# Kernel tuning notes

Hardware: AMD Instinct MI355X
Metric: run time of the kernel (lower is better)

Reference implementation:

```python
import jax, jax.numpy as jnp
import numpy as np

NUM_HEADS = 8
LN_EPS = 1e-5


def setup_inputs() -> dict:
    key = jax.random.key(0)
    ks = jax.random.split(key, 12)
    N, H, G = 100000, 512, 256
    s = 1.0 / np.sqrt(H)
    return {
        "x": jax.random.normal(ks[0], (N, H), dtype=jnp.float32),
        "batch": jnp.sort(jax.random.randint(ks[1], (N,), 0, G)),
        "query": jax.random.normal(ks[2], (H,), dtype=jnp.float32),
        "k_w": jax.random.uniform(ks[3], (H, H), minval=-s, maxval=s, dtype=jnp.float32),
        "k_b": jax.random.uniform(ks[4], (H,), minval=-s, maxval=s, dtype=jnp.float32),
        "v_w": jax.random.uniform(ks[5], (H, H), minval=-s, maxval=s, dtype=jnp.float32),
        "v_b": jax.random.uniform(ks[6], (H,), minval=-s, maxval=s, dtype=jnp.float32),
        "o_w": jax.random.uniform(ks[7], (H, H), minval=-s, maxval=s, dtype=jnp.float32),
        "o_b": jax.random.uniform(ks[8], (H,), minval=-s, maxval=s, dtype=jnp.float32),
        "ln_g": jnp.ones((H,), dtype=jnp.float32),
        "ln_b": jnp.zeros((H,), dtype=jnp.float32),
        "num_graphs": 256,
    }


def reference(x, batch, query, k_w, k_b, v_w, v_b, o_w, o_b, ln_g, ln_b, num_graphs):
    N, H = x.shape
    nh = NUM_HEADS
    hd = H // nh
    # projections (torch Linear: x @ W.T + b)
    k = (x @ k_w.T + k_b).reshape(N, nh, hd)
    v = (x @ v_w.T + v_b).reshape(N, nh, hd)
    q = query.reshape(nh, hd)
    # per-node, per-head attention logits against the shared graph query
    s = jnp.einsum("nhd,hd->nh", k, q) / np.float32(np.sqrt(hd))  # [N, nh]
    # segment softmax over nodes of each graph (stable via segment max)
    s_max = jax.ops.segment_max(s, batch, num_segments=num_graphs)  # [G, nh]
    w = jnp.exp(s - s_max[batch])  # [N, nh]
    denom = jax.ops.segment_sum(w, batch, num_segments=num_graphs)  # [G, nh]
    numer = jax.ops.segment_sum(w[:, :, None] * v, batch, num_segments=num_graphs)  # [G, nh, hd]
    attended = numer / jnp.where(denom > 0, denom, 1.0)[:, :, None]  # zeros for empty graphs
    out = attended.reshape(num_graphs, H)
    out = out @ o_w.T + o_b
    # layer norm over last dim
    mu = out.mean(-1, keepdims=True)
    var = out.var(-1, keepdims=True)
    out = (out - mu) / jnp.sqrt(var + LN_EPS) * ln_g + ln_b
    return out
```

## Files before the change

kernel.cpp:

```cpp
#include <hip/hip_runtime.h>
#include <math.h>

#define H 512
#define NH 8
#define NG 256
#define SPLIT 4

#define WS_QK   0
#define WS_SB   4096
#define WS_SEG  4352
#define WS_VWT  8192
#define WS_OWT  270336
#define WS_TP   532480
#define WS_DP   4726784


__global__ __launch_bounds__(256) void k_setup(
    const int* __restrict__ batch, int N, int* __restrict__ seg,
    const float* __restrict__ k_w, const float* __restrict__ k_b,
    const float* __restrict__ query, float* __restrict__ qk, float* __restrict__ sb,
    const float* __restrict__ vw, const float* __restrict__ ow,
    float* __restrict__ vwt, float* __restrict__ owt) {
  __shared__ float tile[32][33];
  const int b = blockIdx.x;
  if (b < 2) {
    int g = b * 256 + threadIdx.x;
    if (g > NG) return;
    int lo = 0, hi = N;
    while (lo < hi) { int mid = (lo + hi) >> 1; if (batch[mid] < g) lo = mid + 1; else hi = mid; }
    seg[g] = lo;
  } else if (b < 18) {
    int gt = (b - 2) * 256 + threadIdx.x;
    int h = gt >> 9, j = gt & 511;
    float a = 0.f;
#pragma unroll 8
    for (int d = 0; d < 64; ++d)
      a = fmaf(k_w[(size_t)(h * 64 + d) * H + j], query[h * 64 + d], a);
    qk[j * 8 + h] = a * 0.125f;
    if (gt < 8) {
      float s = 0.f;
      for (int d = 0; d < 64; ++d) s = fmaf(k_b[gt * 64 + d], query[gt * 64 + d], s);
      sb[gt] = s * 0.125f;
    }
  } else {
    int bb = b - 18;
    const float* in  = (bb < 256) ? vw  : ow;
    float*       out = (bb < 256) ? vwt : owt;
    int tidx = bb & 255;
    int bx = tidx & 15, by = tidx >> 4;
    int tx = threadIdx.x & 31, ty = threadIdx.x >> 5;
#pragma unroll
    for (int k = 0; k < 4; ++k)
      tile[ty + 8 * k][tx] = in[(size_t)(by * 32 + ty + 8 * k) * H + bx * 32 + tx];
    __syncthreads();
#pragma unroll
    for (int k = 0; k < 4; ++k)
      out[(size_t)(bx * 32 + ty + 8 * k) * H + by * 32 + tx] = tile[tx][ty + 8 * k];
  }
}


#define DPP_ADD(v, ctrl, rmask)                                                   \
  v += __int_as_float(__builtin_amdgcn_update_dpp(0, __float_as_int(v), ctrl,     \
                                                  rmask, 0xf, true))

__global__ __launch_bounds__(256, 2) void k_main(
    const float* __restrict__ x, const float* __restrict__ qk, const float* __restrict__ sb,
    const int* __restrict__ seg, float* __restrict__ T_part, float* __restrict__ den_part) {
  const int g = blockIdx.x >> 2, p = blockIdx.x & (SPLIT - 1);
  const int s0 = seg[g], e0 = seg[g + 1], len = e0 - s0;
  const int na = s0 + (len * p) / SPLIT;
  const int nb = s0 + (len * (p + 1)) / SPLIT;
  const int lane = threadIdx.x & 63, wid = threadIdx.x >> 6;

  float qk_r[8][8];
#pragma unroll
  for (int ci = 0; ci < 8; ++ci) {
    int j = (ci < 4) ? (4 * lane + ci) : (256 + 4 * lane + ci - 4);
    const float4* row = (const float4*)(qk + j * 8);
    float4 q0 = row[0], q1 = row[1];
    qk_r[ci][0] = q0.x; qk_r[ci][1] = q0.y; qk_r[ci][2] = q0.z; qk_r[ci][3] = q0.w;
    qk_r[ci][4] = q1.x; qk_r[ci][5] = q1.y; qk_r[ci][6] = q1.z; qk_r[ci][7] = q1.w;
  }
  float sbr[8];
#pragma unroll
  for (int h = 0; h < 8; ++h) sbr[h] = sb[h];

  float T_r[8][8];
  float den[8];
#pragma unroll
  for (int h = 0; h < 8; ++h) {
    den[h] = 0.f;
#pragma unroll
    for (int ci = 0; ci < 8; ++ci) T_r[h][ci] = 0.f;
  }

  const float4* x4 = (const float4*)x;
  int n = na + wid;
  float4 b0a, b0b, b1a, b1b;
  if (n < nb)     { size_t a = (size_t)n * 128 + lane;       b0a = x4[a]; b0b = x4[a + 64]; }
  if (n + 4 < nb) { size_t a = (size_t)(n + 4) * 128 + lane; b1a = x4[a]; b1b = x4[a + 64]; }

  for (; n < nb; n += 4) {
    float4 b2a, b2b;
    if (n + 8 < nb) { size_t a = (size_t)(n + 8) * 128 + lane; b2a = x4[a]; b2b = x4[a + 64]; }

    float xv[8] = {b0a.x, b0a.y, b0a.z, b0a.w, b0b.x, b0b.y, b0b.z, b0b.w};
    float pp[8] = {0.f, 0.f, 0.f, 0.f, 0.f, 0.f, 0.f, 0.f};
#pragma unroll
    for (int ci = 0; ci < 8; ++ci)
#pragma unroll
      for (int h = 0; h < 8; ++h) pp[h] = fmaf(xv[ci], qk_r[ci][h], pp[h]);

#pragma unroll
    for (int h = 0; h < 8; ++h) DPP_ADD(pp[h], 0x111, 0xf);
#pragma unroll
    for (int h = 0; h < 8; ++h) DPP_ADD(pp[h], 0x112, 0xf);
#pragma unroll
    for (int h = 0; h < 8; ++h) DPP_ADD(pp[h], 0x114, 0xf);
#pragma unroll
    for (int h = 0; h < 8; ++h) DPP_ADD(pp[h], 0x118, 0xf);
#pragma unroll
    for (int h = 0; h < 8; ++h) DPP_ADD(pp[h], 0x142, 0xa);
#pragma unroll
    for (int h = 0; h < 8; ++h) DPP_ADD(pp[h], 0x143, 0xc);

    float w[8];
#pragma unroll
    for (int h = 0; h < 8; ++h) {
      float s = __int_as_float(__builtin_amdgcn_readlane(__float_as_int(pp[h]), 63));
      w[h] = __expf(s + sbr[h]);
      den[h] += w[h];
    }
#pragma unroll
    for (int h = 0; h < 8; ++h)
#pragma unroll
      for (int ci = 0; ci < 8; ++ci) T_r[h][ci] = fmaf(w[h], xv[ci], T_r[h][ci]);

    b0a = b1a; b0b = b1b; b1a = b2a; b1b = b2b;
  }

  __shared__ float T_lds[8][512];
  __shared__ float den_lds[4][8];
  for (int wv = 0; wv < 4; ++wv) {
    if (wid == wv) {
#pragma unroll
      for (int h = 0; h < 8; ++h) {
        float4 v0 = make_float4(T_r[h][0], T_r[h][1], T_r[h][2], T_r[h][3]);
        float4 v1 = make_float4(T_r[h][4], T_r[h][5], T_r[h][6], T_r[h][7]);
        float4* d0 = (float4*)&T_lds[h][4 * lane];
        float4* d1 = (float4*)&T_lds[h][256 + 4 * lane];
        if (wv == 0) { *d0 = v0; *d1 = v1; }
        else {
          float4 o0 = *d0, o1 = *d1;
          o0.x += v0.x; o0.y += v0.y; o0.z += v0.z; o0.w += v0.w;
          o1.x += v1.x; o1.y += v1.y; o1.z += v1.z; o1.w += v1.w;
          *d0 = o0; *d1 = o1;
        }
      }
      if (lane == 0) {
#pragma unroll
        for (int h = 0; h < 8; ++h) den_lds[wv][h] = den[h];
      }
    }
    __syncthreads();
  }
  const int gp = blockIdx.x;
  float4* Tp4 = (float4*)(T_part + (size_t)gp * (NH * H));
  const float4* Tl4 = (const float4*)T_lds;
  for (int k = threadIdx.x; k < NH * H / 4; k += 256) Tp4[k] = Tl4[k];
  if (threadIdx.x < 8) {
    float d = den_lds[0][threadIdx.x] + den_lds[1][threadIdx.x] +
              den_lds[2][threadIdx.x] + den_lds[3][threadIdx.x];
    den_part[gp * 8 + threadIdx.x] = d;
  }
}


__global__ __launch_bounds__(512) void k_epi(
    const float* __restrict__ T_part, const float* __restrict__ den_part,
    const float* __restrict__ vwt, const float* __restrict__ vb,
    const float* __restrict__ owt, const float* __restrict__ ob,
    const float* __restrict__ lng, const float* __restrict__ lnb,
    float* __restrict__ out) {
  const int g0 = blockIdx.x * 2;
  const int t = threadIdx.x;
  __shared__ float Tl[2][NH * H];
  __shared__ float att[2][H];
  __shared__ float den_s[2][8], dinv_s[2][8];
  __shared__ float red[2][2][8];

#pragma unroll
  for (int gi = 0; gi < 2; ++gi) {
    const float4* tp = (const float4*)(T_part + (size_t)(g0 + gi) * SPLIT * (NH * H));
    float4* tl4 = (float4*)Tl[gi];
    for (int k = t; k < NH * H / 4; k += 512) {
      float4 acc = tp[k];
#pragma unroll
      for (int p = 1; p < SPLIT; ++p) {
        float4 v = tp[p * (NH * H / 4) + k];
        acc.x += v.x; acc.y += v.y; acc.z += v.z; acc.w += v.w;
      }
      tl4[k] = acc;
    }
  }
  if (t < 16) {
    int gi = t >> 3, h = t & 7;
    float d = 0.f;
#pragma unroll
    for (int p = 0; p < SPLIT; ++p) d += den_part[((g0 + gi) * SPLIT + p) * 8 + h];
    den_s[gi][h] = d;
    dinv_s[gi][h] = (d > 0.f) ? 1.f / d : 1.f;
  }
  __syncthreads();

  {
    const int h = t >> 6;
    const float* T0 = &Tl[0][h * H];
    const float* T1 = &Tl[1][h * H];
    float a0 = 0.f, a1 = 0.f;
#pragma unroll 8
    for (int j = 0; j < H; ++j) {
      float wv_ = vwt[(size_t)j * H + t];
      a0 = fmaf(T0[j], wv_, a0);
      a1 = fmaf(T1[j], wv_, a1);
    }
    att[0][t] = (a0 + den_s[0][h] * vb[t]) * dinv_s[0][h];
    att[1][t] = (a1 + den_s[1][h] * vb[t]) * dinv_s[1][h];
  }
  __syncthreads();

  float o0 = ob[t], o1 = o0;
#pragma unroll 8
  for (int k = 0; k < H; ++k) {
    float w_ = owt[(size_t)k * H + t];
    o0 = fmaf(att[0][k], w_, o0);
    o1 = fmaf(att[1][k], w_, o1);
  }

  float r10 = o0, r20 = o0 * o0, r11 = o1, r21 = o1 * o1;
#pragma unroll
  for (int m = 1; m < 64; m <<= 1) {
    r10 += __shfl_xor(r10, m, 64); r20 += __shfl_xor(r20, m, 64);
    r11 += __shfl_xor(r11, m, 64); r21 += __shfl_xor(r21, m, 64);
  }
  if ((t & 63) == 0) {
    red[0][0][t >> 6] = r10; red[0][1][t >> 6] = r20;
    red[1][0][t >> 6] = r11; red[1][1][t >> 6] = r21;
  }
  __syncthreads();
  float S10 = 0.f, S20 = 0.f, S11 = 0.f, S21 = 0.f;
#pragma unroll
  for (int w = 0; w < 8; ++w) {
    S10 += red[0][0][w]; S20 += red[0][1][w];
    S11 += red[1][0][w]; S21 += red[1][1][w];
  }
  float mu0 = S10 * (1.f / 512.f), mu1 = S11 * (1.f / 512.f);
  float var0 = S20 * (1.f / 512.f) - mu0 * mu0;
  float var1 = S21 * (1.f / 512.f) - mu1 * mu1;
  float rs0 = rsqrtf(var0 + 1e-5f), rs1 = rsqrtf(var1 + 1e-5f);
  float gg = lng[t], bb = lnb[t];
  out[(size_t)g0 * H + t]       = (o0 - mu0) * rs0 * gg + bb;
  out[(size_t)(g0 + 1) * H + t] = (o1 - mu1) * rs1 * gg + bb;
}


extern "C" void kernel_launch(void* const* d_in, const int* in_sizes, int n_in,
                              void* d_out, int out_size, void* d_ws, size_t ws_size,
                              hipStream_t stream) {
  const float* x     = (const float*)d_in[0];
  const int*   batch = (const int*)d_in[1];
  const float* query = (const float*)d_in[2];
  const float* k_w   = (const float*)d_in[3];
  const float* k_b   = (const float*)d_in[4];
  const float* v_w   = (const float*)d_in[5];
  const float* v_b   = (const float*)d_in[6];
  const float* o_w   = (const float*)d_in[7];
  const float* o_b   = (const float*)d_in[8];
  const float* ln_g  = (const float*)d_in[9];
  const float* ln_b  = (const float*)d_in[10];
  const int N = in_sizes[0] / H;

  float* ws  = (float*)d_ws;
  float* qk  = ws + WS_QK;
  float* sb  = ws + WS_SB;
  int*   seg = (int*)(ws + WS_SEG);
  float* vwt = ws + WS_VWT;
  float* owt = ws + WS_OWT;
  float* Tp  = ws + WS_TP;
  float* dp  = ws + WS_DP;

  hipLaunchKernelGGL(k_setup, dim3(530), dim3(256), 0, stream,
                     batch, N, seg, k_w, k_b, query, qk, sb, v_w, o_w, vwt, owt);
  hipLaunchKernelGGL(k_main, dim3(NG * SPLIT), dim3(256), 0, stream, x, qk, sb, seg, Tp, dp);
  hipLaunchKernelGGL(k_epi, dim3(NG / 2), dim3(512), 0, stream, Tp, dp, vwt, v_b, owt, o_b,
                     ln_g, ln_b, (float*)d_out);
}
```

Baseline: 374.1 us.

## Fuse per-graph attention pooling and epilogue into one kernel per graph

Measured after the change: 341.7 us. 1.09x faster.

```diff
diff --git a/kernel.cpp b/kernel.cpp
--- a/kernel.cpp
+++ b/kernel.cpp
@@ -4,15 +4,12 @@
 #define H 512
 #define NH 8
 #define NG 256
-#define SPLIT 4
 
 #define WS_QK   0
 #define WS_SB   4096
 #define WS_SEG  4352
 #define WS_VWT  8192
 #define WS_OWT  270336
-#define WS_TP   532480
-#define WS_DP   4726784
 
 
 __global__ __launch_bounds__(256) void k_setup(
@@ -64,14 +61,23 @@
   v += __int_as_float(__builtin_amdgcn_update_dpp(0, __float_as_int(v), ctrl,     \
                                                   rmask, 0xf, true))
 
-__global__ __launch_bounds__(256, 2) void k_main(
+__global__ __launch_bounds__(512, 2) void k_graph(
     const float* __restrict__ x, const float* __restrict__ qk, const float* __restrict__ sb,
-    const int* __restrict__ seg, float* __restrict__ T_part, float* __restrict__ den_part) {
-  const int g = blockIdx.x >> 2, p = blockIdx.x & (SPLIT - 1);
-  const int s0 = seg[g], e0 = seg[g + 1], len = e0 - s0;
-  const int na = s0 + (len * p) / SPLIT;
-  const int nb = s0 + (len * (p + 1)) / SPLIT;
-  const int lane = threadIdx.x & 63, wid = threadIdx.x >> 6;
+    const int* __restrict__ seg, const float* __restrict__ vwt, const float* __restrict__ vb,
+    const float* __restrict__ owt, const float* __restrict__ ob,
+    const float* __restrict__ lng, const float* __restrict__ lnb,
+    float* __restrict__ out) {
+  const int g = blockIdx.x;
+  const int t = threadIdx.x;
+  const int lane = t & 63, wid = t >> 6;
+  const int s0 = seg[g], e0 = seg[g + 1];
+
+  __shared__ float TA[8][512];
+  __shared__ float TB[8][512];
+  __shared__ float den_lds[8][8];
+  __shared__ float att[512];
+  __shared__ float den_s[8], dinv_s[8];
+  __shared__ float redA[8], redB[8];
 
   float qk_r[8][8];
 #pragma unroll
@@ -96,14 +102,14 @@
   }
 
   const float4* x4 = (const float4*)x;
-  int n = na + wid;
+  int n = s0 + wid;
   float4 b0a, b0b, b1a, b1b;
-  if (n < nb)     { size_t a = (size_t)n * 128 + lane;       b0a = x4[a]; b0b = x4[a + 64]; }
-  if (n + 4 < nb) { size_t a = (size_t)(n + 4) * 128 + lane; b1a = x4[a]; b1b = x4[a + 64]; }
-
-  for (; n < nb; n += 4) {
+  if (n < e0)     { size_t a = (size_t)n * 128 + lane;       b0a = x4[a]; b0b = x4[a + 64]; }
+  if (n + 8 < e0) { size_t a = (size_t)(n + 8) * 128 + lane; b1a = x4[a]; b1b = x4[a + 64]; }
+
+  for (; n < e0; n += 8) {
     float4 b2a, b2b;
-    if (n + 8 < nb) { size_t a = (size_t)(n + 8) * 128 + lane; b2a = x4[a]; b2b = x4[a + 64]; }
+    if (n + 16 < e0) { size_t a = (size_t)(n + 16) * 128 + lane; b2a = x4[a]; b2b = x4[a + 64]; }
 
     float xv[8] = {b0a.x, b0a.y, b0a.z, b0a.w, b0b.x, b0b.y, b0b.z, b0b.w};
     float pp[8] = {0.f, 0.f, 0.f, 0.f, 0.f, 0.f, 0.f, 0.f};
@@ -140,17 +146,20 @@
     b0a = b1a; b0b = b1b; b1a = b2a; b1b = b2b;
   }
 
-  __shared__ float T_lds[8][512];
-  __shared__ float den_lds[4][8];
-  for (int wv = 0; wv < 4; ++wv) {
-    if (wid == wv) {
+  if (lane == 0) {
+#pragma unroll
+    for (int h = 0; h < 8; ++h) den_lds[wid][h] = den[h];
+  }
+  for (int s = 0; s < 4; ++s) {
+    if (wid == s || wid == s + 4) {
+      float (*T_)[512] = (wid < 4) ? TA : TB;
 #pragma unroll
       for (int h = 0; h < 8; ++h) {
         float4 v0 = make_float4(T_r[h][0], T_r[h][1], T_r[h][2], T_r[h][3]);
         float4 v1 = make_float4(T_r[h][4], T_r[h][5], T_r[h][6], T_r[h][7]);
-        float4* d0 = (float4*)&T_lds[h][4 * lane];
-        float4* d1 = (float4*)&T_lds[h][256 + 4 * lane];
-        if (wv == 0) { *d0 = v0; *d1 = v1; }
+        float4* d0 = (float4*)&T_[h][4 * lane];
+        float4* d1 = (float4*)&T_[h][256 + 4 * lane];
+        if (s == 0) { *d0 = v0; *d1 = v1; }
         else {
           float4 o0 = *d0, o1 = *d1;
           o0.x += v0.x; o0.y += v0.y; o0.z += v0.z; o0.w += v0.w;
@@ -158,110 +167,46 @@
           *d0 = o0; *d1 = o1;
         }
       }
-      if (lane == 0) {
-#pragma unroll
-        for (int h = 0; h < 8; ++h) den_lds[wv][h] = den[h];
-      }
     }
     __syncthreads();
   }
-  const int gp = blockIdx.x;
-  float4* Tp4 = (float4*)(T_part + (size_t)gp * (NH * H));
-  const float4* Tl4 = (const float4*)T_lds;
-  for (int k = threadIdx.x; k < NH * H / 4; k += 256) Tp4[k] = Tl4[k];
-  if (threadIdx.x < 8) {
-    float d = den_lds[0][threadIdx.x] + den_lds[1][threadIdx.x] +
-              den_lds[2][threadIdx.x] + den_lds[3][threadIdx.x];
-    den_part[gp * 8 + threadIdx.x] = d;
-  }
-}
-
-
-__global__ __launch_bounds__(512) void k_epi(
-    const float* __restrict__ T_part, const float* __restrict__ den_part,
-    const float* __restrict__ vwt, const float* __restrict__ vb,
-    const float* __restrict__ owt, const float* __restrict__ ob,
-    const float* __restrict__ lng, const float* __restrict__ lnb,
-    float* __restrict__ out) {
-  const int g0 = blockIdx.x * 2;
-  const int t = threadIdx.x;
-  __shared__ float Tl[2][NH * H];
-  __shared__ float att[2][H];
-  __shared__ float den_s[2][8], dinv_s[2][8];
-  __shared__ float red[2][2][8];
-
-#pragma unroll
-  for (int gi = 0; gi < 2; ++gi) {
-    const float4* tp = (const float4*)(T_part + (size_t)(g0 + gi) * SPLIT * (NH * H));
-    float4* tl4 = (float4*)Tl[gi];
-    for (int k = t; k < NH * H / 4; k += 512) {
-      float4 acc = tp[k];
-#pragma unroll
-      for (int p = 1; p < SPLIT; ++p) {
-        float4 v = tp[p * (NH * H / 4) + k];
-        acc.x += v.x; acc.y += v.y; acc.z += v.z; acc.w += v.w;
-      }
-      tl4[k] = acc;
-    }
-  }
-  if (t < 16) {
-    int gi = t >> 3, h = t & 7;
+#pragma unroll
+  for (int h = 0; h < 8; ++h) TA[h][t] += TB[h][t];
+  if (t < 8) {
     float d = 0.f;
 #pragma unroll
-    for (int p = 0; p < SPLIT; ++p) d += den_part[((g0 + gi) * SPLIT + p) * 8 + h];
-    den_s[gi][h] = d;
-    dinv_s[gi][h] = (d > 0.f) ? 1.f / d : 1.f;
+    for (int w = 0; w < 8; ++w) d += den_lds[w][t];
+    den_s[t] = d;
+    dinv_s[t] = (d > 0.f) ? 1.f / d : 1.f;
   }
   __syncthreads();
 
-  {
-    const int h = t >> 6;
-    const float* T0 = &Tl[0][h * H];
-    const float* T1 = &Tl[1][h * H];
-    float a0 = 0.f, a1 = 0.f;
-#pragma unroll 8
-    for (int j = 0; j < H; ++j) {
-      float wv_ = vwt[(size_t)j * H + t];
-      a0 = fmaf(T0[j], wv_, a0);
-      a1 = fmaf(T1[j], wv_, a1);
-    }
-    att[0][t] = (a0 + den_s[0][h] * vb[t]) * dinv_s[0][h];
-    att[1][t] = (a1 + den_s[1][h] * vb[t]) * dinv_s[1][h];
-  }
+  const int h = t >> 6;
+  const float* Th = TA[h];
+  float a = 0.f;
+#pragma unroll 16
+  for (int j = 0; j < H; ++j)
+    a = fmaf(Th[j], vwt[(size_t)j * H + t], a);
+  att[t] = (a + den_s[h] * vb[t]) * dinv_s[h];
   __syncthreads();
 
-  float o0 = ob[t], o1 = o0;
-#pragma unroll 8
-  for (int k = 0; k < H; ++k) {
-    float w_ = owt[(size_t)k * H + t];
-    o0 = fmaf(att[0][k], w_, o0);
-    o1 = fmaf(att[1][k], w_, o1);
-  }
-
-  float r10 = o0, r20 = o0 * o0, r11 = o1, r21 = o1 * o1;
-#pragma unroll
-  for (int m = 1; m < 64; m <<= 1) {
-    r10 += __shfl_xor(r10, m, 64); r20 += __shfl_xor(r20, m, 64);
-    r11 += __shfl_xor(r11, m, 64); r21 += __shfl_xor(r21, m, 64);
-  }
-  if ((t & 63) == 0) {
-    red[0][0][t >> 6] = r10; red[0][1][t >> 6] = r20;
-    red[1][0][t >> 6] = r11; red[1][1][t >> 6] = r21;
-  }
+  float o = ob[t];
+#pragma unroll 16
+  for (int k = 0; k < H; ++k)
+    o = fmaf(att[k], owt[(size_t)k * H + t], o);
+
+  float r1 = o, r2 = o * o;
+#pragma unroll
+  for (int m = 1; m < 64; m <<= 1) { r1 += __shfl_xor(r1, m, 64); r2 += __shfl_xor(r2, m, 64); }
+  if (lane == 0) { redA[wid] = r1; redB[wid] = r2; }
   __syncthreads();
-  float S10 = 0.f, S20 = 0.f, S11 = 0.f, S21 = 0.f;
-#pragma unroll
-  for (int w = 0; w < 8; ++w) {
-    S10 += red[0][0][w]; S20 += red[0][1][w];
-    S11 += red[1][0][w]; S21 += red[1][1][w];
-  }
-  float mu0 = S10 * (1.f / 512.f), mu1 = S11 * (1.f / 512.f);
-  float var0 = S20 * (1.f / 512.f) - mu0 * mu0;
-  float var1 = S21 * (1.f / 512.f) - mu1 * mu1;
-  float rs0 = rsqrtf(var0 + 1e-5f), rs1 = rsqrtf(var1 + 1e-5f);
-  float gg = lng[t], bb = lnb[t];
-  out[(size_t)g0 * H + t]       = (o0 - mu0) * rs0 * gg + bb;
-  out[(size_t)(g0 + 1) * H + t] = (o1 - mu1) * rs1 * gg + bb;
+  float S1 = 0.f, S2 = 0.f;
+#pragma unroll
+  for (int w = 0; w < 8; ++w) { S1 += redA[w]; S2 += redB[w]; }
+  float mu = S1 * (1.f / 512.f);
+  float var = S2 * (1.f / 512.f) - mu * mu;
+  float rs = rsqrtf(var + 1e-5f);
+  out[(size_t)g * H + t] = (o - mu) * rs * lng[t] + lnb[t];
 }
 
 
@@ -287,12 +232,9 @@
   int*   seg = (int*)(ws + WS_SEG);
   float* vwt = ws + WS_VWT;
   float* owt = ws + WS_OWT;
-  float* Tp  = ws + WS_TP;
-  float* dp  = ws + WS_DP;
 
   hipLaunchKernelGGL(k_setup, dim3(530), dim3(256), 0, stream,
                      batch, N, seg, k_w, k_b, query, qk, sb, v_w, o_w, vwt, owt);
-  hipLaunchKernelGGL(k_main, dim3(NG * SPLIT), dim3(256), 0, stream, x, qk, sb, seg, Tp, dp);
-  hipLaunchKernelGGL(k_epi, dim3(NG / 2), dim3(512), 0, stream, Tp, dp, vwt, v_b, owt, o_b,
-                     ln_g, ln_b, (float*)d_out);
+  hipLaunchKernelGGL(k_graph, dim3(NG), dim3(512), 0, stream,
+                     x, qk, sb, seg, vwt, v_b, owt, o_b, ln_g, ln_b, (float*)d_out);
 }
```
